# Optimization experiments

Hardware: AMD Instinct MI355X
Metric: run time of the kernel (lower is better)

## Reference

```python
import jax, jax.numpy as jnp
import numpy as np

B, L, D = 8, 1024, 1024  # L must equal D for the elementwise sqrt(K) divide to broadcast


def setup_inputs() -> dict:
    key = jax.random.key(0)
    ks = jax.random.split(key, 9)
    # Non-negative inputs/weights/biases so K = x @ Wk.T + bk >= 0 and sqrt(K) is finite.
    rc = jax.random.uniform(ks[0], (B, L, D), dtype=jnp.float32)
    ri = jax.random.uniform(ks[1], (B, L, D), dtype=jnp.float32)
    tc = jax.random.uniform(ks[2], (B, L, D), dtype=jnp.float32)
    scale = 0.02
    Wq = jax.random.uniform(ks[3], (D, D), dtype=jnp.float32) * scale
    Wk = jax.random.uniform(ks[4], (D, D), dtype=jnp.float32) * scale
    Wv = jax.random.uniform(ks[5], (D, D), dtype=jnp.float32) * scale
    bq = jax.random.uniform(ks[6], (D,), dtype=jnp.float32) * scale
    bk = jax.random.uniform(ks[7], (D,), dtype=jnp.float32) * scale
    bv = jax.random.uniform(ks[8], (D,), dtype=jnp.float32) * scale
    return {
        "reference_caption": rc,
        "reference_image": ri,
        "target_caption": tc,
        "Wq": Wq, "bq": bq,
        "Wk": Wk, "bk": bk,
        "Wv": Wv, "bv": bv,
    }


def reference(reference_caption, reference_image, target_caption, Wq, bq, Wk, bk, Wv, bv):
    # torch nn.Linear: y = x @ W.T + b
    Q = reference_caption @ Wq.T + bq          # [B, Lq, D]
    K = reference_image @ Wk.T + bk            # [B, Lk, D]
    V = reference_image @ Wv.T + bv            # [B, Lk, D]
    matmul_qk = jnp.einsum("bqd,bkd->bqk", Q, K)  # [B, Lq, Lk]
    # Faithful to source: elementwise divide by sqrt(K) tensor (broadcasts since Lq==Lk==D).
    scaled_logits = matmul_qk / jnp.sqrt(K)
    attention_weights = jax.nn.softmax(scaled_logits, axis=-1)
    output = jnp.einsum("bqk,bkd->bqd", attention_weights, V)
    return (output, attention_weights)
```

## Files before the change

kernel.cpp:

```cpp
#include <hip/hip_runtime.h>
#include <hip/hip_fp16.h>
#include <math.h>

typedef unsigned short u16;
typedef __attribute__((ext_vector_type(8))) _Float16 half8;
typedef __attribute__((ext_vector_type(4))) float f32x4;

#define ASLOT 4096
#define SLOT  12288

__device__ __forceinline__ u16 f2h(float f){ __half h=__float2half(f); u16 r; __builtin_memcpy(&r,&h,2); return r; }
__device__ __forceinline__ float h2f(u16 u){ __half h; __builtin_memcpy(&h,&u,2); return __half2float(h); }

template<int ROWS, bool WRAP>
__device__ __forceinline__ void stage_tile(const u16* __restrict__ G, int rowbase, int ldg,
                                           int k0, u16* Ls, int tid){
#pragma unroll
    for (int p = 0; p < ROWS / 64; ++p){
        const int lin = tid + p * 256;
        const int row = lin >> 2;
        const int cg  = ((lin & 3) ^ ((row >> 1) & 3)) * 8;
        const int kk  = WRAP ? (k0 & 1023) : k0;
        const u16* g = G + (size_t)(rowbase + row) * ldg + (kk + cg);
        __builtin_amdgcn_global_load_lds(
            (__attribute__((address_space(1))) void*)g,
            (__attribute__((address_space(3))) void*)(Ls + (size_t)lin * 8), 16, 0, 0);
    }
}

template<int EPI, int BIASM, bool AWRAP>
__device__ __forceinline__ void gemm_core(
    const u16* __restrict__ A, const u16* __restrict__ B,
    const float* __restrict__ bias,
    float* __restrict__ of, u16* __restrict__ oh,
    int by, int bx, int lda, int ldb, int ldc, int K, u16* sh)
{
    const int tid  = threadIdx.x;
    const int lane = tid & 63, wv = tid >> 6;
    const int wr = (wv >> 1) * 64;
    const int wc = (wv & 1) * 128;
    const int row0 = by * 128, col0 = bx * 256;
    const int lr = lane & 15, hi = lane >> 4;
    const int co = (hi ^ ((lr >> 1) & 3)) * 8;

    f32x4 acc[4][8];
#pragma unroll
    for (int m = 0; m < 4; m++)
#pragma unroll
        for (int n = 0; n < 8; n++) acc[m][n] = (f32x4){0.f, 0.f, 0.f, 0.f};

    auto stage_set = [&](int buf, int k0){
        u16* s = sh + buf * SLOT;
        stage_tile<128, AWRAP>(A, row0, lda, k0, s, tid);
        stage_tile<256, false>(B, col0, ldb, k0, s + ASLOT, tid);
    };

    const int NIT = K >> 5;
    stage_set(0, 0);
    stage_set(1, 32);
    int bufs = 2, bufr = 0;
    for (int t = 0; t < NIT; ++t){
        if (t + 2 < NIT){ stage_set(bufs, (t + 2) << 5); bufs = (bufs + 1 == 3) ? 0 : bufs + 1; }
        const int rem = NIT - 1 - t;
        if (rem >= 2)      asm volatile("s_waitcnt vmcnt(12)" ::: "memory");
        else if (rem == 1) asm volatile("s_waitcnt vmcnt(6)" ::: "memory");
        else               asm volatile("s_waitcnt vmcnt(0)" ::: "memory");
        __builtin_amdgcn_s_barrier();
        __builtin_amdgcn_sched_barrier(0);

        const u16* s = sh + bufr * SLOT;
        bufr = (bufr + 1 == 3) ? 0 : bufr + 1;

        half8 a[4], b[8];
#pragma unroll
        for (int m = 0; m < 4; m++) a[m] = *(const half8*)&s[(wr + m * 16 + lr) * 32 + co];
#pragma unroll
        for (int n = 0; n < 8; n++) b[n] = *(const half8*)&s[ASLOT + (wc + n * 16 + lr) * 32 + co];
#pragma unroll
        for (int m = 0; m < 4; m++)
#pragma unroll
            for (int n = 0; n < 8; n++)
                acc[m][n] = __builtin_amdgcn_mfma_f32_16x16x32_f16(a[m], b[n], acc[m][n], 0, 0, 0);
        __builtin_amdgcn_sched_barrier(0);
        __builtin_amdgcn_s_barrier();
    }

#pragma unroll
    for (int m = 0; m < 4; m++) {
        const int rb = row0 + wr + m * 16 + hi * 4;
#pragma unroll
        for (int n = 0; n < 8; n++) {
            const int c = col0 + wc + n * 16 + lr;
            const float bc = (BIASM == 1) ? bias[c] : 0.f;
#pragma unroll
            for (int q = 0; q < 4; q++) {
                const int r = rb + q;
                float v = acc[m][n][q] + bc;
                if (BIASM == 2) v += bias[r];
                const size_t idx = (size_t)r * ldc + c;
                if (EPI == 0) of[idx] = v;
                else if (EPI == 1) oh[idx] = f2h(v);
                else { const u16 hh = f2h(v); oh[idx] = hh; oh[idx + 1024] = f2h(v - h2f(hh)); }
            }
        }
    }
}

__global__ __launch_bounds__(256, 2) void lin_qk_k(
    const u16* __restrict__ rc_h, const u16* __restrict__ ri_h,
    const u16* __restrict__ Wq_h, const u16* __restrict__ Wk_h,
    const float* __restrict__ bq, const float* __restrict__ bk,
    u16* __restrict__ Q_h, u16* __restrict__ Kcat)
{
    __shared__ __align__(16) u16 sh[3 * SLOT];
    const int nwg = gridDim.x, chunk = nwg >> 3;
    const int swz = ((int)blockIdx.x & 7) * chunk + ((int)blockIdx.x >> 3);
    const int p = swz & 1, t = swz >> 1;
    if (p == 0) {
        gemm_core<1, 1, false>(rc_h, Wq_h, bq, nullptr, Q_h,
                               t >> 2, t & 3, 1024, 1024, 1024, 1024, sh);
    } else {
        gemm_core<2, 1, false>(ri_h, Wk_h, bk, nullptr, Kcat,
                               t >> 2, t & 3, 1024, 1024, 2048, 1024, sh);
    }
}

__global__ __launch_bounds__(256, 2) void qkt_vt_k(
    const u16* __restrict__ Q_h, const u16* __restrict__ Kcat,
    const u16* __restrict__ ri_h, const u16* __restrict__ Wv_h,
    const float* __restrict__ bv,
    float* __restrict__ wts, u16* __restrict__ Vt)
{
    __shared__ __align__(16) u16 sh[3 * SLOT];
    const int nwg = gridDim.x, chunk = nwg >> 3;
    const int swz = ((int)blockIdx.x & 7) * chunk + ((int)blockIdx.x >> 3);
    const int p = swz & 1, t = swz >> 1;
    if (p == 0) {
        const int z = t >> 5, rem = t & 31;
        gemm_core<0, 0, true>(Q_h + (size_t)z * 1048576, Kcat + (size_t)z * 2097152,
                              nullptr, wts + (size_t)z * 1048576, nullptr,
                              rem >> 2, rem & 3, 1024, 2048, 1024, 2048, sh);
    } else {
        gemm_core<1, 2, false>(Wv_h, ri_h, bv, nullptr, Vt,
                               t >> 5, t & 31, 1024, 1024, 8192, 1024, sh);
    }
}

__global__ __launch_bounds__(256, 2) void av_k(
    const u16* __restrict__ W_h, const u16* __restrict__ Vt, float* __restrict__ outp)
{
    __shared__ __align__(16) u16 sh[3 * SLOT];
    const int nwg = gridDim.x, chunk = nwg >> 3;
    const int wg = ((int)blockIdx.x & 7) * chunk + ((int)blockIdx.x >> 3);
    const int z = wg >> 5, rem = wg & 31;
    gemm_core<0, 0, false>(W_h + (size_t)z * 1048576, Vt + (size_t)z * 1024,
                           nullptr, outp + (size_t)z * 1048576, nullptr,
                           rem >> 2, rem & 3, 1024, 8192, 1024, 1024, sh);
}

__global__ __launch_bounds__(256)
void softmax_scale_k(float* __restrict__ W, const u16* __restrict__ Kcat, u16* __restrict__ Wh)
{
    const long row = blockIdx.x;
    float* p = W + (row << 10);
    const int tid = threadIdx.x;

    float4 v = ((const float4*)p)[tid];
    const ushort4 kh = ((const ushort4*)(Kcat + (row << 11)))[tid];
    const ushort4 kl = ((const ushort4*)(Kcat + (row << 11) + 1024))[tid];
    v.x *= rsqrtf(h2f(kh.x) + h2f(kl.x));
    v.y *= rsqrtf(h2f(kh.y) + h2f(kl.y));
    v.z *= rsqrtf(h2f(kh.z) + h2f(kl.z));
    v.w *= rsqrtf(h2f(kh.w) + h2f(kl.w));

    float m = fmaxf(fmaxf(v.x, v.y), fmaxf(v.z, v.w));
#pragma unroll
    for (int o = 32; o >= 1; o >>= 1) m = fmaxf(m, __shfl_xor(m, o));
    __shared__ float sm[4];
    const int wid = tid >> 6, lane = tid & 63;
    if (lane == 0) sm[wid] = m;
    __syncthreads();
    m = fmaxf(fmaxf(sm[0], sm[1]), fmaxf(sm[2], sm[3]));

    v.x = __expf(v.x - m); v.y = __expf(v.y - m);
    v.z = __expf(v.z - m); v.w = __expf(v.w - m);
    float s = v.x + v.y + v.z + v.w;
#pragma unroll
    for (int o = 32; o >= 1; o >>= 1) s += __shfl_xor(s, o);
    __shared__ float ss[4];
    if (lane == 0) ss[wid] = s;
    __syncthreads();
    s = ss[0] + ss[1] + ss[2] + ss[3];

    const float inv = 1.0f / s;
    v.x *= inv; v.y *= inv; v.z *= inv; v.w *= inv;
    ((float4*)p)[tid] = v;

    ushort4 ub;
    ub.x = f2h(v.x); ub.y = f2h(v.y); ub.z = f2h(v.z); ub.w = f2h(v.w);
    ((ushort4*)(Wh + (row << 10)))[tid] = ub;
}

__global__ __launch_bounds__(256)
void conv_plain5_k(const float4* __restrict__ x0, ushort4* __restrict__ y0,
                   const float4* __restrict__ x1, ushort4* __restrict__ y1,
                   const float4* __restrict__ x2, ushort4* __restrict__ y2,
                   const float4* __restrict__ x3, ushort4* __restrict__ y3,
                   const float4* __restrict__ x4, ushort4* __restrict__ y4)
{
    const long i = (long)blockIdx.x * 256 + threadIdx.x;
    const long n0 = 2097152, n1 = 262144;
    const float4* x; ushort4* y; long j;
    if (i < n0)                 { x = x0; y = y0; j = i; }
    else if (i < 2*n0)          { x = x1; y = y1; j = i - n0; }
    else if (i < 2*n0 + n1)     { x = x2; y = y2; j = i - 2*n0; }
    else if (i < 2*n0 + 2*n1)   { x = x3; y = y3; j = i - 2*n0 - n1; }
    else                        { x = x4; y = y4; j = i - 2*n0 - 2*n1; }
    const float4 v = x[j];
    ushort4 o;
    o.x = f2h(v.x); o.y = f2h(v.y); o.z = f2h(v.z); o.w = f2h(v.w);
    y[j] = o;
}

extern "C" void kernel_launch(void* const* d_in, const int* in_sizes, int n_in,
                              void* d_out, int out_size, void* d_ws, size_t ws_size,
                              hipStream_t stream)
{
    const float* rc = (const float*)d_in[0];
    const float* ri = (const float*)d_in[1];
    const float* Wq = (const float*)d_in[3];
    const float* bq = (const float*)d_in[4];
    const float* Wk = (const float*)d_in[5];
    const float* bk = (const float*)d_in[6];
    const float* Wv = (const float*)d_in[7];
    const float* bv = (const float*)d_in[8];

    const long M8 = 8192 * 1024L;
    const long M1 = 1024 * 1024L;

    u16* ws   = (u16*)d_ws;
    u16* ri_h = ws;
    u16* rc_h = ws + 1 * M8;
    u16* Kcat = ws + 2 * M8;
    u16* Wq_h = ws + 4 * M8;
    u16* Wk_h = Wq_h + M1;
    u16* Wv_h = Wk_h + M1;

    float* outp = (float*)d_out;
    float* wts  = outp + M8;
    u16*   Q_h  = (u16*)d_out;
    u16*   Vt   = rc_h;
    u16*   W_h  = ri_h;

    conv_plain5_k<<<19456, 256, 0, stream>>>(
        (const float4*)ri, (ushort4*)ri_h, (const float4*)rc, (ushort4*)rc_h,
        (const float4*)Wq, (ushort4*)Wq_h, (const float4*)Wk, (ushort4*)Wk_h,
        (const float4*)Wv, (ushort4*)Wv_h);

    lin_qk_k<<<512, 256, 0, stream>>>(rc_h, ri_h, Wq_h, Wk_h, bq, bk, Q_h, Kcat);

    qkt_vt_k<<<512, 256, 0, stream>>>(Q_h, Kcat, ri_h, Wv_h, bv, wts, Vt);

    softmax_scale_k<<<8192, 256, 0, stream>>>(wts, Kcat, W_h);

    av_k<<<256, 256, 0, stream>>>(W_h, Vt, outp);
}
```

Baseline: 164.7 us.

## Center K by column mean to halve the QK^T contraction length

Replaces the hi/lo fp16 split of K, which doubled the QK^T contraction to 2048, with a mean-centered K (Kd = K - column mean) stored as a single fp16 value. The dropped term is added back as a per-row bias u = Q·cm. That bias comes from new small kernels: a column-mean reduction with atomics and two row-dot kernels, plus a memset. The aim is to halve the QK^T GEMM work. In exchange it adds several extra launches, an extra 16MB Kd write in the K projection epilogue, and relies on centering to keep fp16 precision acceptable.

```diff
diff --git a/kernel.cpp b/kernel.cpp
--- a/kernel.cpp
+++ b/kernel.cpp
@@ -12,7 +12,7 @@
 __device__ __forceinline__ u16 f2h(float f){ __half h=__float2half(f); u16 r; __builtin_memcpy(&r,&h,2); return r; }
 __device__ __forceinline__ float h2f(u16 u){ __half h; __builtin_memcpy(&h,&u,2); return __half2float(h); }
 
-template<int ROWS, bool WRAP>
+template<int ROWS>
 __device__ __forceinline__ void stage_tile(const u16* __restrict__ G, int rowbase, int ldg,
                                            int k0, u16* Ls, int tid){
 #pragma unroll
@@ -20,19 +20,19 @@
         const int lin = tid + p * 256;
         const int row = lin >> 2;
         const int cg  = ((lin & 3) ^ ((row >> 1) & 3)) * 8;
-        const int kk  = WRAP ? (k0 & 1023) : k0;
-        const u16* g = G + (size_t)(rowbase + row) * ldg + (kk + cg);
+        const u16* g = G + (size_t)(rowbase + row) * ldg + (k0 + cg);
         __builtin_amdgcn_global_load_lds(
             (__attribute__((address_space(1))) void*)g,
             (__attribute__((address_space(3))) void*)(Ls + (size_t)lin * 8), 16, 0, 0);
     }
 }
 
-template<int EPI, int BIASM, bool AWRAP>
+template<int EPI, int BIASM>
 __device__ __forceinline__ void gemm_core(
     const u16* __restrict__ A, const u16* __restrict__ B,
     const float* __restrict__ bias,
     float* __restrict__ of, u16* __restrict__ oh,
+    const float* __restrict__ cm, u16* __restrict__ od,
     int by, int bx, int lda, int ldb, int ldc, int K, u16* sh)
 {
     const int tid  = threadIdx.x;
@@ -51,8 +51,8 @@
 
     auto stage_set = [&](int buf, int k0){
         u16* s = sh + buf * SLOT;
-        stage_tile<128, AWRAP>(A, row0, lda, k0, s, tid);
-        stage_tile<256, false>(B, col0, ldb, k0, s + ASLOT, tid);
+        stage_tile<128>(A, row0, lda, k0, s, tid);
+        stage_tile<256>(B, col0, ldb, k0, s + ASLOT, tid);
     };
 
     const int NIT = K >> 5;
@@ -100,7 +100,12 @@
                 const size_t idx = (size_t)r * ldc + c;
                 if (EPI == 0) of[idx] = v;
                 else if (EPI == 1) oh[idx] = f2h(v);
-                else { const u16 hh = f2h(v); oh[idx] = hh; oh[idx + 1024] = f2h(v - h2f(hh)); }
+                else {
+                    const u16 hh = f2h(v);
+                    oh[idx] = hh; oh[idx + 1024] = f2h(v - h2f(hh));
+                    if (EPI == 3)
+                        od[(size_t)r * 1024 + c] = f2h(v - cm[(size_t)((r >> 10) << 10) + c]);
+                }
             }
         }
     }
@@ -110,25 +115,26 @@
     const u16* __restrict__ rc_h, const u16* __restrict__ ri_h,
     const u16* __restrict__ Wq_h, const u16* __restrict__ Wk_h,
     const float* __restrict__ bq, const float* __restrict__ bk,
-    u16* __restrict__ Q_h, u16* __restrict__ Kcat)
+    const float* __restrict__ cm,
+    u16* __restrict__ Q_h, u16* __restrict__ Kcat, u16* __restrict__ Kd)
 {
     __shared__ __align__(16) u16 sh[3 * SLOT];
     const int nwg = gridDim.x, chunk = nwg >> 3;
     const int swz = ((int)blockIdx.x & 7) * chunk + ((int)blockIdx.x >> 3);
     const int p = swz & 1, t = swz >> 1;
     if (p == 0) {
-        gemm_core<1, 1, false>(rc_h, Wq_h, bq, nullptr, Q_h,
-                               t >> 2, t & 3, 1024, 1024, 1024, 1024, sh);
+        gemm_core<1, 1>(rc_h, Wq_h, bq, nullptr, Q_h, nullptr, nullptr,
+                        t >> 2, t & 3, 1024, 1024, 1024, 1024, sh);
     } else {
-        gemm_core<2, 1, false>(ri_h, Wk_h, bk, nullptr, Kcat,
-                               t >> 2, t & 3, 1024, 1024, 2048, 1024, sh);
+        gemm_core<3, 1>(ri_h, Wk_h, bk, nullptr, Kcat, cm, Kd,
+                        t >> 2, t & 3, 1024, 1024, 2048, 1024, sh);
     }
 }
 
 __global__ __launch_bounds__(256, 2) void qkt_vt_k(
-    const u16* __restrict__ Q_h, const u16* __restrict__ Kcat,
+    const u16* __restrict__ Q_h, const u16* __restrict__ Kd,
     const u16* __restrict__ ri_h, const u16* __restrict__ Wv_h,
-    const float* __restrict__ bv,
+    const float* __restrict__ bv, const float* __restrict__ u,
     float* __restrict__ wts, u16* __restrict__ Vt)
 {
     __shared__ __align__(16) u16 sh[3 * SLOT];
@@ -137,12 +143,13 @@
     const int p = swz & 1, t = swz >> 1;
     if (p == 0) {
         const int z = t >> 5, rem = t & 31;
-        gemm_core<0, 0, true>(Q_h + (size_t)z * 1048576, Kcat + (size_t)z * 2097152,
-                              nullptr, wts + (size_t)z * 1048576, nullptr,
-                              rem >> 2, rem & 3, 1024, 2048, 1024, 2048, sh);
+        gemm_core<0, 2>(Q_h + ((size_t)z << 20), Kd + ((size_t)z << 20),
+                        u + ((size_t)z << 10), wts + ((size_t)z << 20), nullptr,
+                        nullptr, nullptr,
+                        rem >> 2, rem & 3, 1024, 1024, 1024, 1024, sh);
     } else {
-        gemm_core<1, 2, false>(Wv_h, ri_h, bv, nullptr, Vt,
-                               t >> 5, t & 31, 1024, 1024, 8192, 1024, sh);
+        gemm_core<1, 2>(Wv_h, ri_h, bv, nullptr, Vt, nullptr, nullptr,
+                        t >> 5, t & 31, 1024, 1024, 8192, 1024, sh);
     }
 }
 
@@ -153,9 +160,41 @@
     const int nwg = gridDim.x, chunk = nwg >> 3;
     const int wg = ((int)blockIdx.x & 7) * chunk + ((int)blockIdx.x >> 3);
     const int z = wg >> 5, rem = wg & 31;
-    gemm_core<0, 0, false>(W_h + (size_t)z * 1048576, Vt + (size_t)z * 1024,
-                           nullptr, outp + (size_t)z * 1048576, nullptr,
-                           rem >> 2, rem & 3, 1024, 8192, 1024, 1024, sh);
+    gemm_core<0, 0>(W_h + ((size_t)z << 20), Vt + (size_t)z * 1024,
+                    nullptr, outp + ((size_t)z << 20), nullptr, nullptr, nullptr,
+                    rem >> 2, rem & 3, 1024, 8192, 1024, 1024, sh);
+}
+
+__global__ __launch_bounds__(256)
+void colmean_k(const u16* __restrict__ ri_h, float* __restrict__ xbar)
+{
+    const int b = blockIdx.x >> 5, sub = blockIdx.x & 31;
+    const int dg = sub & 3, rg = sub >> 2;
+    const int d = dg * 256 + threadIdx.x;
+    const u16* base = ri_h + ((size_t)b << 20) + ((size_t)(rg * 128) << 10) + d;
+    float s = 0.f;
+#pragma unroll 4
+    for (int r = 0; r < 128; ++r) s += h2f(base[(size_t)r << 10]);
+    atomicAdd(&xbar[(b << 10) + d], s * (1.f / 1024.f));
+}
+
+template<bool BIAS, bool AFULL>
+__global__ __launch_bounds__(256)
+void rowdot_k(const u16* __restrict__ A, const float* __restrict__ B,
+              const float* __restrict__ bias, float* __restrict__ out)
+{
+    const int o = blockIdx.x * 4 + (threadIdx.x >> 6);
+    const int lane = threadIdx.x & 63;
+    const int ar = AFULL ? o : (o & 1023);
+    const int br = o >> 10;
+    const u16* ap = A + ((size_t)ar << 10);
+    const float* bp = B + ((size_t)br << 10);
+    float s = 0.f;
+#pragma unroll
+    for (int j = 0; j < 16; ++j){ const int i = lane + (j << 6); s += h2f(ap[i]) * bp[i]; }
+#pragma unroll
+    for (int off = 32; off >= 1; off >>= 1) s += __shfl_xor(s, off);
+    if (lane == 0) out[o] = s + (BIAS ? bias[ar] : 0.f);
 }
 
 __global__ __launch_bounds__(256)
@@ -242,9 +281,13 @@
     u16* ri_h = ws;
     u16* rc_h = ws + 1 * M8;
     u16* Kcat = ws + 2 * M8;
-    u16* Wq_h = ws + 4 * M8;
+    u16* Kd   = ws + 4 * M8;
+    u16* Wq_h = ws + 5 * M8;
     u16* Wk_h = Wq_h + M1;
     u16* Wv_h = Wk_h + M1;
+    float* xbar = (float*)(ws + 5 * M8 + 3 * M1);
+    float* cm   = xbar + 8192;
+    float* uu   = cm + 8192;
 
     float* outp = (float*)d_out;
     float* wts  = outp + M8;
@@ -257,9 +300,16 @@
         (const float4*)Wq, (ushort4*)Wq_h, (const float4*)Wk, (ushort4*)Wk_h,
         (const float4*)Wv, (ushort4*)Wv_h);
 
-    lin_qk_k<<<512, 256, 0, stream>>>(rc_h, ri_h, Wq_h, Wk_h, bq, bk, Q_h, Kcat);
-
-    qkt_vt_k<<<512, 256, 0, stream>>>(Q_h, Kcat, ri_h, Wv_h, bv, wts, Vt);
+    hipMemsetAsync(xbar, 0, 8192 * sizeof(float), stream);
+    colmean_k<<<256, 256, 0, stream>>>(ri_h, xbar);
+
+    rowdot_k<true, false><<<2048, 256, 0, stream>>>(Wk_h, xbar, bk, cm);
+
+    lin_qk_k<<<512, 256, 0, stream>>>(rc_h, ri_h, Wq_h, Wk_h, bq, bk, cm, Q_h, Kcat, Kd);
+
+    rowdot_k<false, true><<<2048, 256, 0, stream>>>(Q_h, cm, nullptr, uu);
+
+    qkt_vt_k<<<512, 256, 0, stream>>>(Q_h, Kd, ri_h, Wv_h, bv, uu, wts, Vt);
 
     softmax_scale_k<<<8192, 256, 0, stream>>>(wts, Kcat, W_h);
 
```

New measurement: 167.2 us. Within noise of the previous version (+1.5%).
